# Performance work log

Measured on AMD Instinct MI355X. Metric: run time of the kernel, lower is better.

## Reference

```python
import jax, jax.numpy as jnp
import numpy as np

HEADS = 4
HEAD_DIM = 32
DIM = 256
EPS = 1e-12  # F.normalize eps


def setup_inputs() -> dict:
    key = jax.random.key(0)
    ks = jax.random.split(key, 5)
    inner = HEADS * HEAD_DIM
    x = jax.random.normal(ks[0], (4, DIM, 64, 64), dtype=jnp.float32)
    g = jax.random.normal(ks[1], (DIM,), dtype=jnp.float32) * 0.02 + 1.0  # RMSNorm gain
    w_qkv = jax.random.normal(ks[2], (3 * inner, DIM), dtype=jnp.float32) * (DIM ** -0.5)
    w_out = jax.random.normal(ks[3], (DIM, inner), dtype=jnp.float32) * (inner ** -0.5)
    b_out = jax.random.normal(ks[4], (DIM,), dtype=jnp.float32) * 0.01
    return {"x": x, "g": g, "w_qkv": w_qkv, "w_out": w_out, "b_out": b_out}


def reference(x, g, w_qkv, w_out, b_out):
    b, c, h, w = x.shape
    n = h * w
    # RMSNorm over channel dim: F.normalize(x, dim=1) * g * sqrt(dim)
    xn = x * jax.lax.rsqrt(jnp.mean(x * x, axis=1, keepdims=True) + EPS) * g[None, :, None, None]
    # 1x1 conv QKV (no bias): [b, 3*heads*head_dim, h, w]
    qkv = jnp.einsum('bchw,oc->bohw', xn, w_qkv)
    q, k, v = jnp.split(qkv, 3, axis=1)

    def to_bhnd(t):
        # [b, heads*head_dim, h, w] -> [b, heads, n, head_dim]
        return t.reshape(b, HEADS, HEAD_DIM, n).transpose(0, 1, 3, 2)

    q, k, v = to_bhnd(q), to_bhnd(k), to_bhnd(v)
    scale = HEAD_DIM ** -0.5
    sim = jnp.einsum('bhid,bhjd->bhij', q, k) * scale  # [b, heads, n, n]
    attn = jax.nn.softmax(sim, axis=-1)
    out = jnp.einsum('bhij,bhjd->bhid', attn, v)  # [b, heads, n, head_dim]
    # [b, heads, n, head_dim] -> [b, heads*head_dim, h, w]
    out = out.transpose(0, 1, 3, 2).reshape(b, HEADS * HEAD_DIM, h, w)
    # 1x1 conv output projection with bias
    return jnp.einsum('bchw,oc->bohw', out, w_out) + b_out[None, :, None, None]
```

## Files before the change

kernel.cpp:

```cpp
#include <hip/hip_runtime.h>
#include <hip/hip_bf16.h>
#include <stdint.h>
#include <stddef.h>

typedef __attribute__((ext_vector_type(8))) short short8;
typedef __attribute__((ext_vector_type(4))) float f32x4;
typedef __attribute__((ext_vector_type(16))) float f32x16;
typedef __attribute__((ext_vector_type(4))) unsigned int uint4v;

#define MFMA16(a, b, c) __builtin_amdgcn_mfma_f32_16x16x32_bf16((a), (b), (c), 0, 0, 0)
#define MFMA32(a, b, c) __builtin_amdgcn_mfma_f32_32x32x16_bf16((a), (b), (c), 0, 0, 0)

__device__ __forceinline__ unsigned short f2bf(float f) {
  unsigned int u = __builtin_bit_cast(unsigned int, f);
  u += 0x7fffu + ((u >> 16) & 1u);
  return (unsigned short)(u >> 16);
}

__device__ __forceinline__ unsigned int pk2(float lo, float hi) {
  return (unsigned int)f2bf(lo) | ((unsigned int)f2bf(hi) << 16);
}

__device__ __forceinline__ unsigned int pkc(float lo, float hi) {
  __hip_bfloat162 h = __float22bfloat162_rn(make_float2(lo, hi));
  unsigned int u;
  __builtin_memcpy(&u, &h, 4);
  return u;
}

__device__ __forceinline__ short8 mk8(const unsigned short* p) {
  return *(const short8*)p;
}

__device__ __forceinline__ f32x16 zero16() {
  f32x16 v;
#pragma unroll
  for (int i = 0; i < 16; ++i) v[i] = 0.f;
  return v;
}

__device__ __forceinline__ int swz40(int row, int c) {
  return row * 40 + ((((c >> 3) ^ (row >> 3)) & 3) << 3) + (c & 7);
}

__global__ __launch_bounds__(256) void k_prep(const float* __restrict__ wq,
                                              const float* __restrict__ wo,
                                              unsigned short* __restrict__ wq_bf,
                                              unsigned short* __restrict__ wo_bf) {
  int i = blockIdx.x * 256 + threadIdx.x;
  if (i < 98304) wq_bf[i] = f2bf(wq[i]);
  if (i < 32768) wo_bf[i] = f2bf(wo[i]);
}

__global__ __launch_bounds__(256) void k_qkv(const float* __restrict__ x,
                                             const float* __restrict__ g,
                                             const unsigned short* __restrict__ wq_bf,
                                             unsigned short* __restrict__ qbuf,
                                             unsigned short* __restrict__ kbuf,
                                             unsigned short* __restrict__ vbuf) {
  int bid = blockIdx.x;
  int b = bid / 192;
  int rem = bid % 192;
  int ot = rem / 32;
  int pt = rem % 32;
  int o0 = ot * 64, p0 = pt * 128;

  __shared__ unsigned short xnT[2][128 * 40];
  __shared__ float sqv[8][128];
  __shared__ float rl[128];

  int t = threadIdx.x;
  int lane = t & 63, w = t >> 6;
  int lr = lane & 15, lg = lane >> 4;
  int pq = t & 31;
  int cp = t >> 5;

  const float* xb = x + (size_t)b * 256 * 4096;
  const unsigned short* wqrow = wq_bf + (size_t)(o0 + w * 16 + lr) * 256;

  f32x4 acc[8];
  f32x4 z = {0.f, 0.f, 0.f, 0.f};
#pragma unroll
  for (int i = 0; i < 8; ++i) acc[i] = z;
  f32x4 sacc = z;

#define STAGE_CHUNK(buf, c0)                                                   \
  {                                                                            \
    _Pragma("unroll")                                                          \
    for (int s = 0; s < 2; ++s) {                                              \
      int cb = (c0) + s * 16 + cp * 2;                                         \
      f32x4 xa = *(const f32x4*)&xb[(size_t)cb * 4096 + p0 + pq * 4];          \
      f32x4 xc = *(const f32x4*)&xb[(size_t)(cb + 1) * 4096 + p0 + pq * 4];    \
      float ga = g[cb], gc = g[cb + 1];                                        \
      int cloc = s * 16 + cp * 2;                                              \
      _Pragma("unroll")                                                        \
      for (int k = 0; k < 4; ++k) {                                            \
        sacc[k] += xa[k] * xa[k] + xc[k] * xc[k];                              \
        *(unsigned int*)&xnT[buf][swz40(pq * 4 + k, cloc)] =                   \
            pkc(xa[k] * ga, xc[k] * gc);                                       \
      }                                                                        \
    }                                                                          \
  }

  STAGE_CHUNK(0, 0)
  __syncthreads();

  for (int cc = 0; cc < 8; ++cc) {
    int cur = cc & 1;
    if (cc < 7) STAGE_CHUNK(cur ^ 1, (cc + 1) * 32)
    short8 af = mk8(wqrow + cc * 32 + lg * 8);
#pragma unroll
    for (int pt16 = 0; pt16 < 8; ++pt16) {
      short8 bf = mk8(&xnT[cur][swz40(pt16 * 16 + lr, lg * 8)]);
      acc[pt16] = MFMA16(af, bf, acc[pt16]);
    }
    __syncthreads();
  }
#undef STAGE_CHUNK

#pragma unroll
  for (int k = 0; k < 4; ++k) sqv[cp][pq * 4 + k] = sacc[k];
  __syncthreads();
  if (t < 128) {
    float tot = 0.f;
#pragma unroll
    for (int r = 0; r < 8; ++r) tot += sqv[r][t];
    rl[t] = rsqrtf(tot * (1.0f / 256.0f) + 1e-12f);
  }
  __syncthreads();

  const float cexp = 0.25505654427102996f;
  int obase = o0 + w * 16 + lg * 4;
  if (obase < 128) {
    int h = obase >> 5, d0 = obase & 31;
    unsigned short* dst = qbuf + ((size_t)(b * 4 + h) * 4096) * 32;
#pragma unroll
    for (int pt16 = 0; pt16 < 8; ++pt16) {
      int p = p0 + pt16 * 16 + lr;
      float rr = rl[pt16 * 16 + lr];
      unsigned int u0 = pk2(acc[pt16][0] * rr, acc[pt16][1] * rr);
      unsigned int u1 = pk2(acc[pt16][2] * rr, acc[pt16][3] * rr);
      uint2 uu = {u0, u1};
      *(uint2*)(dst + (size_t)p * 32 + d0) = uu;
    }
  } else if (obase < 256) {
    int oh = obase - 128;
    int h = oh >> 5, d0 = oh & 31;
    int frag = d0 >> 4, hi = (d0 >> 3) & 1, i0 = d0 & 7;
    unsigned short* dst = kbuf + (size_t)(b * 4 + h) * 131072
                         + frag * 512 + hi * 256 + i0;
#pragma unroll
    for (int pt16 = 0; pt16 < 8; ++pt16) {
      int jj = p0 + pt16 * 16 + lr;
      float rr = rl[pt16 * 16 + lr] * cexp;
      int jtile = jj >> 5, j31 = jj & 31;
      uint2 uu = {pk2(acc[pt16][0] * rr, acc[pt16][1] * rr),
                  pk2(acc[pt16][2] * rr, acc[pt16][3] * rr)};
      *(uint2*)(dst + (size_t)jtile * 1024 + j31 * 8) = uu;
    }
  } else {
    int oh = obase - 256;
    int h = oh >> 5, d0 = oh & 31;
    unsigned short* dst = vbuf + (size_t)(b * 4 + h) * 131072;
    int sl = (lr & 3) | ((lr & 4) << 1) | ((lr & 8) >> 1);
#pragma unroll
    for (int pt16 = 0; pt16 < 8; ++pt16) {
      int jj = p0 + pt16 * 16 + sl;
      float rr = rl[pt16 * 16 + lr];
      int jtile = jj >> 5, j5 = jj & 31;
      int frag = j5 >> 4, hi = (j5 >> 3) & 1, i = j5 & 7;
      size_t base = (size_t)jtile * 1024 + frag * 512 + hi * 256 + i;
#pragma unroll
      for (int r = 0; r < 4; ++r)
        dst[base + (d0 + r) * 8] = f2bf(acc[pt16][r] * rr);
    }
  }
}

__device__ __forceinline__ void attn_tile(short8 kf0, short8 kf1, short8 vf0, short8 vf1,
                                          short8 qf0, short8 qf1, short8 onesf,
                                          const f32x16& z16,
                                          f32x16& lsacc, f32x16& oacc) {
  f32x16 s = MFMA32(kf0, qf0, z16);
  s = MFMA32(kf1, qf1, s);

  float p[16];
#pragma unroll
  for (int i = 0; i < 16; ++i) p[i] = __builtin_amdgcn_exp2f(s[i]);

  uint4v u0 = {pkc(p[0], p[1]), pkc(p[2], p[3]), pkc(p[4], p[5]), pkc(p[6], p[7])};
  uint4v u1 = {pkc(p[8], p[9]), pkc(p[10], p[11]), pkc(p[12], p[13]), pkc(p[14], p[15])};
  short8 pf0 = __builtin_bit_cast(short8, u0);
  short8 pf1 = __builtin_bit_cast(short8, u1);

  lsacc = MFMA32(onesf, pf0, lsacc);
  lsacc = MFMA32(onesf, pf1, lsacc);
  oacc = MFMA32(vf0, pf0, oacc);
  oacc = MFMA32(vf1, pf1, oacc);
}

__global__ __launch_bounds__(256, 4) void k_attn(const unsigned short* __restrict__ qbuf,
                                                 const unsigned short* __restrict__ kbuf,
                                                 const unsigned short* __restrict__ vbuf,
                                                 unsigned short* __restrict__ attno) {
  __shared__ float Ol[3][16][64];
  __shared__ float Ll[3][64];

  int bid = blockIdx.x;
  int wid = ((bid & 7) << 8) | (bid >> 3);
  int qg = wid & 127, bh = wid >> 7;
  int t = threadIdx.x, lane = t & 63, jq = t >> 6;
  int l31 = lane & 31, hi = lane >> 5;

  const unsigned short* qgp = qbuf + (size_t)bh * 4096 * 32;
  const unsigned short* kt = kbuf + (size_t)bh * 131072;
  const unsigned short* vt = vbuf + (size_t)bh * 131072;

  int qrow = qg * 32 + l31;
  short8 qf0 = mk8(qgp + (size_t)qrow * 32 + hi * 8);
  short8 qf1 = mk8(qgp + (size_t)qrow * 32 + 16 + hi * 8);

  unsigned int one2 = 0x3F803F80u;
  uint4v ov = {one2, one2, one2, one2};
  short8 onesf = __builtin_bit_cast(short8, ov);

  const f32x16 z16 = zero16();
  f32x16 oacc = zero16();
  f32x16 lsacc = zero16();

  const unsigned short* kpA = kt + (size_t)(jq * 32) * 1024 + lane * 8;
  const unsigned short* vpA = vt + (size_t)(jq * 32) * 1024 + lane * 8;
  const unsigned short* kpB = kpA + 1024;
  const unsigned short* vpB = vpA + 1024;

  short8 kA0 = mk8(kpA), kA1 = mk8(kpA + 512);
  short8 vA0 = mk8(vpA), vA1 = mk8(vpA + 512);
  short8 kB0 = mk8(kpB), kB1 = mk8(kpB + 512);
  short8 vB0 = mk8(vpB), vB1 = mk8(vpB + 512);
  kpA += 2048; vpA += 2048;
  kpB += 2048; vpB += 2048;

  for (int it = 0; it < 16; ++it) {
    attn_tile(kA0, kA1, vA0, vA1, qf0, qf1, onesf, z16, lsacc, oacc);
    kA0 = mk8(kpA);
    kA1 = mk8(kpA + 512);
    vA0 = mk8(vpA);
    vA1 = mk8(vpA + 512);
    kpA += 2048; vpA += 2048;

    attn_tile(kB0, kB1, vB0, vB1, qf0, qf1, onesf, z16, lsacc, oacc);
    kB0 = mk8(kpB);
    kB1 = mk8(kpB + 512);
    vB0 = mk8(vpB);
    vB1 = mk8(vpB + 512);
    kpB += 2048; vpB += 2048;
  }

  float lsum = lsacc[0];

  if (jq > 0) {
#pragma unroll
    for (int i = 0; i < 16; ++i) Ol[jq - 1][i][lane] = oacc[i];
    Ll[jq - 1][lane] = lsum;
  }
  __syncthreads();
  if (jq == 0) {
    float rinv = 1.0f / (lsum + Ll[0][lane] + Ll[1][lane] + Ll[2][lane]);

    int b = bh >> 2, h = bh & 3;
    unsigned short* ob = attno + ((size_t)b * 4096 + qrow) * 128 + h * 32;
#pragma unroll
    for (int r2 = 0; r2 < 8; ++r2) {
      int reg = r2 * 2;
      int dv = (reg & 3) + 8 * (reg >> 2) + 4 * hi;
      float v0 = (oacc[reg] + Ol[0][reg][lane] + Ol[1][reg][lane] + Ol[2][reg][lane]) * rinv;
      float v1 = (oacc[reg + 1] + Ol[0][reg + 1][lane] + Ol[1][reg + 1][lane] + Ol[2][reg + 1][lane]) * rinv;
      *(unsigned int*)(ob + dv) = pk2(v0, v1);
    }
  }
}

__global__ __launch_bounds__(256) void k_out(const unsigned short* __restrict__ attno,
                                             const unsigned short* __restrict__ wo_bf,
                                             const float* __restrict__ bo,
                                             float* __restrict__ out) {
  int bid = blockIdx.x;
  int b = bid >> 8;
  int rem = bid & 255;
  int cog = rem >> 6;
  int p0 = (rem & 63) * 64;
  int co0 = cog * 64;
  int t = threadIdx.x, lane = t & 63, w = t >> 6;
  int lr = lane & 15, lg = lane >> 4;

  f32x4 z = {0.f, 0.f, 0.f, 0.f};
  f32x4 acc[4];
#pragma unroll
  for (int j = 0; j < 4; ++j) acc[j] = z;

  for (int c0 = 0; c0 < 128; c0 += 32) {
    short8 afr = mk8(wo_bf + (size_t)(co0 + w * 16 + lr) * 128 + c0 + lg * 8);
#pragma unroll
    for (int pt16 = 0; pt16 < 4; ++pt16) {
      short8 bfr = mk8(attno + (size_t)(b * 4096 + p0 + pt16 * 16 + lr) * 128 + c0 + lg * 8);
      acc[pt16] = MFMA16(afr, bfr, acc[pt16]);
    }
  }

#pragma unroll
  for (int pt16 = 0; pt16 < 4; ++pt16) {
#pragma unroll
    for (int r = 0; r < 4; ++r) {
      int co = co0 + w * 16 + lg * 4 + r;
      int p = p0 + pt16 * 16 + lr;
      out[((size_t)b * 256 + co) * 4096 + p] = acc[pt16][r] + bo[co];
    }
  }
}

extern "C" void kernel_launch(void* const* d_in, const int* in_sizes, int n_in,
                              void* d_out, int out_size, void* d_ws, size_t ws_size,
                              hipStream_t stream) {
  const float* x = (const float*)d_in[0];
  const float* g = (const float*)d_in[1];
  const float* wq = (const float*)d_in[2];
  const float* wo = (const float*)d_in[3];
  const float* bo = (const float*)d_in[4];
  float* out = (float*)d_out;

  char* ws = (char*)d_ws;
  unsigned short* wq_bf = (unsigned short*)(ws + 65536);
  unsigned short* wo_bf = (unsigned short*)(ws + 262144);
  unsigned short* qbuf = (unsigned short*)(ws + 327680);
  unsigned short* kbuf = (unsigned short*)(ws + 4521984);
  unsigned short* vbuf = (unsigned short*)(ws + 8716288);
  unsigned short* attno = (unsigned short*)(ws + 12910592);

  k_prep<<<dim3(384), dim3(256), 0, stream>>>(wq, wo, wq_bf, wo_bf);
  k_qkv<<<dim3(768), dim3(256), 0, stream>>>(x, g, wq_bf, qbuf, kbuf, vbuf);
  k_attn<<<dim3(2048), dim3(256), 0, stream>>>(qbuf, kbuf, vbuf, attno);
  k_out<<<dim3(1024), dim3(256), 0, stream>>>(attno, wo_bf, bo, out);
}
```

Baseline: 99.81 us.

## Process two query tiles per attention block and compute row sums with VALU adds

Each attention block now covers 64 query rows as two 32-row sub-tiles that share the same K/V fragments. This halves K/V global loads per query and halves the grid size. The softmax denominator is now built with scalar adds plus a cross-half shuffle instead of extra MFMAs against a ones matrix, which removes a third of the matrix ops per tile. In exchange it raises register pressure (two output accumulators), doubles the LDS used for the reduction, and leaves fewer blocks to hide latency.

After: 119.8 us. 20.0% more time.

```diff
diff --git a/kernel.cpp b/kernel.cpp
--- a/kernel.cpp
+++ b/kernel.cpp
@@ -30,6 +30,10 @@
 
 __device__ __forceinline__ short8 mk8(const unsigned short* p) {
   return *(const short8*)p;
+}
+
+__device__ __forceinline__ float redsum32(float v) {
+  return v + __shfl_xor(v, 32);
 }
 
 __device__ __forceinline__ f32x16 zero16() {
@@ -177,24 +181,25 @@
   }
 }
 
-__device__ __forceinline__ void attn_tile(short8 kf0, short8 kf1, short8 vf0, short8 vf1,
-                                          short8 qf0, short8 qf1, short8 onesf,
-                                          const f32x16& z16,
-                                          f32x16& lsacc, f32x16& oacc) {
+__device__ __forceinline__ void attn_sub(short8 kf0, short8 kf1, short8 vf0, short8 vf1,
+                                         short8 qf0, short8 qf1,
+                                         const f32x16& z16, float& lsum, f32x16& oacc) {
   f32x16 s = MFMA32(kf0, qf0, z16);
   s = MFMA32(kf1, qf1, s);
 
   float p[16];
 #pragma unroll
   for (int i = 0; i < 16; ++i) p[i] = __builtin_amdgcn_exp2f(s[i]);
+
+  float s0 = ((p[0] + p[1]) + (p[2] + p[3])) + ((p[4] + p[5]) + (p[6] + p[7]));
+  float s1 = ((p[8] + p[9]) + (p[10] + p[11])) + ((p[12] + p[13]) + (p[14] + p[15]));
+  lsum += s0 + s1;
 
   uint4v u0 = {pkc(p[0], p[1]), pkc(p[2], p[3]), pkc(p[4], p[5]), pkc(p[6], p[7])};
   uint4v u1 = {pkc(p[8], p[9]), pkc(p[10], p[11]), pkc(p[12], p[13]), pkc(p[14], p[15])};
   short8 pf0 = __builtin_bit_cast(short8, u0);
   short8 pf1 = __builtin_bit_cast(short8, u1);
 
-  lsacc = MFMA32(onesf, pf0, lsacc);
-  lsacc = MFMA32(onesf, pf1, lsacc);
   oacc = MFMA32(vf0, pf0, oacc);
   oacc = MFMA32(vf1, pf1, oacc);
 }
@@ -203,12 +208,12 @@
                                                  const unsigned short* __restrict__ kbuf,
                                                  const unsigned short* __restrict__ vbuf,
                                                  unsigned short* __restrict__ attno) {
-  __shared__ float Ol[3][16][64];
-  __shared__ float Ll[3][64];
+  __shared__ float Ol[3][2][16][64];
+  __shared__ float Ll[3][2][64];
 
   int bid = blockIdx.x;
-  int wid = ((bid & 7) << 8) | (bid >> 3);
-  int qg = wid & 127, bh = wid >> 7;
+  int wid = ((bid & 7) << 7) | (bid >> 3);
+  int qg = wid & 63, bh = wid >> 6;
   int t = threadIdx.x, lane = t & 63, jq = t >> 6;
   int l31 = lane & 31, hi = lane >> 5;
 
@@ -216,17 +221,17 @@
   const unsigned short* kt = kbuf + (size_t)bh * 131072;
   const unsigned short* vt = vbuf + (size_t)bh * 131072;
 
-  int qrow = qg * 32 + l31;
-  short8 qf0 = mk8(qgp + (size_t)qrow * 32 + hi * 8);
-  short8 qf1 = mk8(qgp + (size_t)qrow * 32 + 16 + hi * 8);
-
-  unsigned int one2 = 0x3F803F80u;
-  uint4v ov = {one2, one2, one2, one2};
-  short8 onesf = __builtin_bit_cast(short8, ov);
+  int qrowA = qg * 64 + l31;
+  int qrowB = qrowA + 32;
+  short8 qA0 = mk8(qgp + (size_t)qrowA * 32 + hi * 8);
+  short8 qA1 = mk8(qgp + (size_t)qrowA * 32 + 16 + hi * 8);
+  short8 qB0 = mk8(qgp + (size_t)qrowB * 32 + hi * 8);
+  short8 qB1 = mk8(qgp + (size_t)qrowB * 32 + 16 + hi * 8);
 
   const f32x16 z16 = zero16();
-  f32x16 oacc = zero16();
-  f32x16 lsacc = zero16();
+  f32x16 oaccA = zero16();
+  f32x16 oaccB = zero16();
+  float lsumA = 0.f, lsumB = 0.f;
 
   const unsigned short* kpA = kt + (size_t)(jq * 32) * 1024 + lane * 8;
   const unsigned short* vpA = vt + (size_t)(jq * 32) * 1024 + lane * 8;
@@ -241,14 +246,16 @@
   kpB += 2048; vpB += 2048;
 
   for (int it = 0; it < 16; ++it) {
-    attn_tile(kA0, kA1, vA0, vA1, qf0, qf1, onesf, z16, lsacc, oacc);
+    attn_sub(kA0, kA1, vA0, vA1, qA0, qA1, z16, lsumA, oaccA);
+    attn_sub(kA0, kA1, vA0, vA1, qB0, qB1, z16, lsumB, oaccB);
     kA0 = mk8(kpA);
     kA1 = mk8(kpA + 512);
     vA0 = mk8(vpA);
     vA1 = mk8(vpA + 512);
     kpA += 2048; vpA += 2048;
 
-    attn_tile(kB0, kB1, vB0, vB1, qf0, qf1, onesf, z16, lsacc, oacc);
+    attn_sub(kB0, kB1, vB0, vB1, qA0, qA1, z16, lsumA, oaccA);
+    attn_sub(kB0, kB1, vB0, vB1, qB0, qB1, z16, lsumB, oaccB);
     kB0 = mk8(kpB);
     kB1 = mk8(kpB + 512);
     vB0 = mk8(vpB);
@@ -256,26 +263,36 @@
     kpB += 2048; vpB += 2048;
   }
 
-  float lsum = lsacc[0];
+  lsumA = redsum32(lsumA);
+  lsumB = redsum32(lsumB);
 
   if (jq > 0) {
 #pragma unroll
-    for (int i = 0; i < 16; ++i) Ol[jq - 1][i][lane] = oacc[i];
-    Ll[jq - 1][lane] = lsum;
+    for (int i = 0; i < 16; ++i) {
+      Ol[jq - 1][0][i][lane] = oaccA[i];
+      Ol[jq - 1][1][i][lane] = oaccB[i];
+    }
+    Ll[jq - 1][0][lane] = lsumA;
+    Ll[jq - 1][1][lane] = lsumB;
   }
   __syncthreads();
   if (jq == 0) {
-    float rinv = 1.0f / (lsum + Ll[0][lane] + Ll[1][lane] + Ll[2][lane]);
-
     int b = bh >> 2, h = bh & 3;
-    unsigned short* ob = attno + ((size_t)b * 4096 + qrow) * 128 + h * 32;
-#pragma unroll
-    for (int r2 = 0; r2 < 8; ++r2) {
-      int reg = r2 * 2;
-      int dv = (reg & 3) + 8 * (reg >> 2) + 4 * hi;
-      float v0 = (oacc[reg] + Ol[0][reg][lane] + Ol[1][reg][lane] + Ol[2][reg][lane]) * rinv;
-      float v1 = (oacc[reg + 1] + Ol[0][reg + 1][lane] + Ol[1][reg + 1][lane] + Ol[2][reg + 1][lane]) * rinv;
-      *(unsigned int*)(ob + dv) = pk2(v0, v1);
+#pragma unroll
+    for (int qs = 0; qs < 2; ++qs) {
+      float lsum = qs ? lsumB : lsumA;
+      const f32x16& oacc = qs ? oaccB : oaccA;
+      float rinv = 1.0f / (lsum + Ll[0][qs][lane] + Ll[1][qs][lane] + Ll[2][qs][lane]);
+      int qrow = qs ? qrowB : qrowA;
+      unsigned short* ob = attno + ((size_t)b * 4096 + qrow) * 128 + h * 32;
+#pragma unroll
+      for (int r2 = 0; r2 < 8; ++r2) {
+        int reg = r2 * 2;
+        int dv = (reg & 3) + 8 * (reg >> 2) + 4 * hi;
+        float v0 = (oacc[reg] + Ol[0][qs][reg][lane] + Ol[1][qs][reg][lane] + Ol[2][qs][reg][lane]) * rinv;
+        float v1 = (oacc[reg + 1] + Ol[0][qs][reg + 1][lane] + Ol[1][qs][reg + 1][lane] + Ol[2][qs][reg + 1][lane]) * rinv;
+        *(unsigned int*)(ob + dv) = pk2(v0, v1);
+      }
     }
   }
 }
@@ -338,6 +355,6 @@
 
   k_prep<<<dim3(384), dim3(256), 0, stream>>>(wq, wo, wq_bf, wo_bf);
   k_qkv<<<dim3(768), dim3(256), 0, stream>>>(x, g, wq_bf, qbuf, kbuf, vbuf);
-  k_attn<<<dim3(2048), dim3(256), 0, stream>>>(qbuf, kbuf, vbuf, attno);
+  k_attn<<<dim3(1024), dim3(256), 0, stream>>>(qbuf, kbuf, vbuf, attno);
   k_out<<<dim3(1024), dim3(256), 0, stream>>>(attno, wo_bf, bo, out);
 }
```
